# Kernel tuning notes

Hardware: AMD Instinct MI355X
Metric: run time of the kernel (lower is better)

Reference implementation:

```python
import jax, jax.numpy as jnp
import numpy as np

D_MODEL, D_HEAD, N_HEAD = 1024, 64, 16
B, T1, T2 = 2, 2048, 2048


def setup_inputs() -> dict:
    key = jax.random.key(0)
    ks = jax.random.split(key, 8)
    s = 1.0 / np.sqrt(D_MODEL)
    return {
        "x": jax.random.normal(ks[0], (B, T1, D_MODEL), dtype=jnp.float32),
        "context": jax.random.normal(ks[1], (B, T2, D_MODEL), dtype=jnp.float32),
        "bias": jax.random.normal(ks[2], (T1, T2), dtype=jnp.float32),
        "W_q": jax.random.normal(ks[3], (D_MODEL, N_HEAD * D_HEAD), dtype=jnp.float32) * s,
        "W_k": jax.random.normal(ks[4], (D_MODEL, N_HEAD * D_HEAD), dtype=jnp.float32) * s,
        "W_v": jax.random.normal(ks[5], (D_MODEL, N_HEAD * D_HEAD), dtype=jnp.float32) * s,
        "W_out": jax.random.normal(ks[6], (N_HEAD * D_HEAD, D_MODEL), dtype=jnp.float32) * s,
        "b_out": jnp.zeros((D_MODEL,), dtype=jnp.float32),
    }


def reference(x, context, bias, W_q, W_k, W_v, W_out, b_out):
    Bq, T1_, _ = x.shape
    T2_ = context.shape[1]
    atten_scale = 1.0 / np.sqrt(D_HEAD)
    # fixed (non-trainable) per-head scale: 2^{-1}, ..., 2^{-n_head}
    head_scale = jnp.exp2(-jnp.arange(1, N_HEAD + 1, dtype=jnp.float32))

    # projections -> [B, H, T, d]
    q = (x @ W_q).reshape(Bq, T1_, N_HEAD, D_HEAD).transpose(0, 2, 1, 3)
    k = (context @ W_k).reshape(Bq, T2_, N_HEAD, D_HEAD).transpose(0, 2, 1, 3)
    v = (context @ W_v).reshape(Bq, T2_, N_HEAD, D_HEAD).transpose(0, 2, 1, 3)

    # scores: [B, H, T1, T2]
    scores = jnp.einsum("bhqd,bhkd->bhqk", q, k) * atten_scale
    scores = scores + bias[None, None, :, :] * head_scale[None, :, None, None]
    attn = jax.nn.softmax(scores, axis=-1)

    out = jnp.einsum("bhqk,bhkd->bqhd", attn, v).reshape(Bq, T1_, N_HEAD * D_HEAD)
    # dropout is identity in eval mode
    return out @ W_out + b_out
```

## Files before the change

kernel.cpp:

```cpp
#include <hip/hip_runtime.h>

typedef float  f32x4   __attribute__((ext_vector_type(4)));
typedef float  f32x16  __attribute__((ext_vector_type(16)));
typedef __bf16 bf16x8  __attribute__((ext_vector_type(8)));
typedef __bf16 bf16x2  __attribute__((ext_vector_type(2)));
typedef short  short8v __attribute__((ext_vector_type(8)));
typedef unsigned uint4v __attribute__((ext_vector_type(4)));

__device__ __forceinline__ short f2bf(float f) {
  unsigned u = __float_as_uint(f);
  unsigned r = (u + 0x7FFFu + ((u >> 16) & 1u)) >> 16;
  return (short)r;
}

__device__ __forceinline__ float exp2_native(float x) {
#if __has_builtin(__builtin_amdgcn_exp2f)
  return __builtin_amdgcn_exp2f(x);
#else
  float r;
  asm("v_exp_f32 %0, %1" : "=v"(r) : "v"(x));
  return r;
#endif
}

__device__ __forceinline__ f32x4 mfma16(bf16x8 a, bf16x8 b, f32x4 c) {
  return __builtin_amdgcn_mfma_f32_16x16x32_bf16(a, b, c, 0, 0, 0);
}
__device__ __forceinline__ f32x16 mfma32(bf16x8 a, bf16x8 b, f32x16 c) {
  return __builtin_amdgcn_mfma_f32_32x32x16_bf16(a, b, c, 0, 0, 0);
}

__device__ __forceinline__ void gload16(const void* g, void* l) {
  __builtin_amdgcn_global_load_lds(
      (const __attribute__((address_space(1))) unsigned int*)g,
      (__attribute__((address_space(3))) unsigned int*)l,
      16, 0, 0);
}

__device__ __forceinline__ bf16x8 p_exchange(const unsigned* pk, int a, int hi) {
  unsigned y1 = hi ? pk[4 * a + 0] : pk[4 * a + 2];
  unsigned z1 = __shfl_xor(y1, 32);
  unsigned y2 = hi ? pk[4 * a + 1] : pk[4 * a + 3];
  unsigned z2 = __shfl_xor(y2, 32);
  unsigned w0 = hi ? z1 : pk[4 * a + 0];
  unsigned w1 = hi ? z2 : pk[4 * a + 1];
  unsigned w2 = hi ? pk[4 * a + 2] : z1;
  unsigned w3 = hi ? pk[4 * a + 3] : z2;
  uint4v q4 = {w0, w1, w2, w3};
  return __builtin_bit_cast(bf16x8, q4);
}


__global__ __launch_bounds__(256) void cvt_copy(const float* __restrict__ in,
                                                short* __restrict__ out, int n4) {
  int i = blockIdx.x * blockDim.x + threadIdx.x;
  int stride = gridDim.x * blockDim.x;
  for (; i < n4; i += stride) {
    float4 v = *(const float4*)&in[i * 4];
    short4 o;
    o.x = f2bf(v.x); o.y = f2bf(v.y); o.z = f2bf(v.z); o.w = f2bf(v.w);
    *(short4*)&out[i * 4] = o;
  }
}

__global__ __launch_bounds__(256) void cvt_bias_frag(const float* __restrict__ bias,
                                                     short* __restrict__ frag) {
  __shared__ short lb[2][2][64][8];
  int kt = blockIdx.x, w4 = blockIdx.y, Qi = blockIdx.z;
  int t = threadIdx.x;
  int row = t >> 3;
  int c0 = (t & 7) * 8;
  const float* src = bias + (size_t)(Qi * 128 + w4 * 32 + row) * 2048 + kt * 64 + c0;
  float4 v0 = *(const float4*)(src + 0);
  float4 v1 = *(const float4*)(src + 4);
  float vv[8] = {v0.x, v0.y, v0.z, v0.w, v1.x, v1.y, v1.z, v1.w};
#pragma unroll
  for (int j = 0; j < 8; j++) {
    int kc64 = c0 + j;
    int s = kc64 >> 5, kc5 = kc64 & 31;
    int hi = (kc5 >> 2) & 1, a = kc5 & 3, bq = kc5 >> 3;
    int half = bq >> 1, idx = a + 4 * (bq & 1);
    lb[s][half][hi * 32 + row][idx] = f2bf(vv[j]);
  }
  __syncthreads();
  short8v val = ((const short8v*)&lb[0][0][0][0])[t];
  size_t base = ((size_t)((Qi * 4 + w4) * 32 + kt)) * 2048;
  *(short8v*)&frag[base + t * 8] = val;
}

__global__ __launch_bounds__(256) void cvt_transpose4(const float* __restrict__ W0,
                                                      const float* __restrict__ W1,
                                                      const float* __restrict__ W2,
                                                      const float* __restrict__ W3,
                                                      short* __restrict__ T0,
                                                      short* __restrict__ T1,
                                                      short* __restrict__ T2,
                                                      short* __restrict__ T3) {
  __shared__ short t_s[64][72];
  int z = blockIdx.z;
  const float* W = (z == 0) ? W0 : (z == 1) ? W1 : (z == 2) ? W2 : W3;
  short* Wt = (z == 0) ? T0 : (z == 1) ? T1 : (z == 2) ? T2 : T3;
  int k0 = blockIdx.y * 64, n0 = blockIdx.x * 64;
  int tid = threadIdx.x;
#pragma unroll
  for (int i = 0; i < 4; i++) {
    int idx = i * 256 + tid;
    int r = idx >> 4, cg = idx & 15;
    float4 v = *(const float4*)&W[(k0 + r) * 1024 + n0 + cg * 4];
    t_s[cg * 4 + 0][r] = f2bf(v.x);
    t_s[cg * 4 + 1][r] = f2bf(v.y);
    t_s[cg * 4 + 2][r] = f2bf(v.z);
    t_s[cg * 4 + 3][r] = f2bf(v.w);
  }
  __syncthreads();
#pragma unroll
  for (int i = 0; i < 2; i++) {
    int idx = i * 256 + tid;
    int r = idx >> 3, cg = idx & 7;
    short8v val = *(short8v*)&t_s[r][cg * 8];
    *(short8v*)&Wt[(n0 + r) * 1024 + k0 + cg * 8] = val;
  }
}

template <int EPI>
__global__ __launch_bounds__(256, 4) void gemm_bf16(const short* __restrict__ A,
                                                    const short* __restrict__ Bt,
                                                    void* __restrict__ out,
                                                    void* __restrict__ out2,
                                                    const float* __restrict__ bout) {
  constexpr int KD = 1024;
  constexpr int NB = (EPI == 3) ? 32 : 16;
  __shared__ short a_s[64][64];
  __shared__ short b_s[64][64];
  int tid = threadIdx.x, w = tid >> 6, lane = tid & 63;
  int g = lane >> 4, c16 = lane & 15;
  int hsw = c16 & 7;

  int lin = blockIdx.x + NB * blockIdx.y;
  int wk = (lin & 7) * (NB * 8) + (lin >> 3);
  int c0 = (wk & (NB - 1)) * 64, r0 = (wk / NB) * 64;

  int wr = (w >> 1) * 32, wc = (w & 1) * 32;
  f32x4 acc[2][2] = {};

  for (int kt = 0; kt < KD / 64; ++kt) {
    int k0 = kt * 64;
    __syncthreads();
#pragma unroll
    for (int i = 0; i < 2; i++) {
      int cb = i * 256 + w * 64;
      int c = cb + lane;
      int row = c >> 3, kg = c & 7;
      int sw = (kg ^ (row & 7)) * 8;
      gload16(A + (r0 + row) * KD + k0 + sw, (char*)a_s + cb * 16);
      gload16(Bt + (c0 + row) * KD + k0 + sw, (char*)b_s + cb * 16);
    }
    __syncthreads();
#pragma unroll
    for (int kk = 0; kk < 2; kk++) {
      bf16x8 af[2], bf[2];
      int sl0 = ((4 * kk + g) ^ hsw) * 8;
#pragma unroll
      for (int m = 0; m < 2; m++) af[m] = *(const bf16x8*)&a_s[wr + m * 16 + c16][sl0];
#pragma unroll
      for (int n = 0; n < 2; n++) bf[n] = *(const bf16x8*)&b_s[wc + n * 16 + c16][sl0];
#pragma unroll
      for (int m = 0; m < 2; m++)
#pragma unroll
        for (int n = 0; n < 2; n++) acc[m][n] = mfma16(af[m], bf[n], acc[m][n]);
    }
  }

#pragma unroll
  for (int m = 0; m < 2; m++)
#pragma unroll
    for (int n = 0; n < 2; n++)
#pragma unroll
      for (int r = 0; r < 4; r++) {
        int row = r0 + wr + m * 16 + g * 4 + r;
        int col = c0 + wc + n * 16 + c16;
        float v = acc[m][n][r];
        int b = row >> 11, t = row & 2047;
        if (EPI == 2) {
          ((float*)out)[row * 1024 + col] = v + bout[col];
        } else if (EPI == 0) {
          int h = col >> 6, d = col & 63;
          ((short*)out)[(((b * 16 + h) * 2048) + t) * 64 + d] = f2bf(v);
        } else {
          if (col < 1024) {
            int h = col >> 6, d = col & 63;
            ((short*)out)[(((b * 16 + h) * 2048) + t) * 64 + d] = f2bf(v);
          } else {
            int cv = col - 1024;
            int h = cv >> 6, d = cv & 63;
            ((short*)out2)[(((b * 16 + h) * 64) + d) * 2048 + t] = f2bf(v);
          }
        }
      }
}

__global__ __launch_bounds__(512, 4) void flash_attn(const short* __restrict__ Qg,
                                                     const short* __restrict__ Kg,
                                                     const short* __restrict__ Vtg,
                                                     const short* __restrict__ bfrag,
                                                     short* __restrict__ Og) {
  __shared__ short k_s[2][2][64][64];
  __shared__ short v_s[2][2][64][64];

  int tid = threadIdx.x, w = tid >> 6, lane = tid & 63;
  int gid = w >> 2, w4 = w & 3;
  int hi = lane >> 5, ll = lane & 31, l7 = ll & 7;

  int lin = blockIdx.x + 16 * (blockIdx.y + 16 * blockIdx.z);
  int wk = (lin & 7) * 64 + (lin >> 3);
  int Qi = wk & 15;
  int qb = Qi * 128;
  int h = (wk >> 4) & 15;
  int b = wk >> 8;

  const short* Qh = Qg + (size_t)(b * 16 + h) * 2048 * 64;
  const short* Kh = Kg + (size_t)(b * 16 + h) * 2048 * 64;
  const short* Vh = Vtg + (size_t)(b * 16 + h) * 64 * 2048;

  const float C1 = 0.125f * 1.44269504f;
  const float C2 = exp2f(-(float)(h + 1)) * 1.44269504f;

  int qrow = qb + w4 * 32 + ll;
  const short* bw = bfrag + ((size_t)(Qi * 4 + w4) * 32) * 2048 + lane * 8;

  int srow = tid >> 3, st8 = tid & 7;
  int ssw = (st8 ^ (srow & 7)) * 8;

  {
    gload16(Kh + srow * 64 + ssw, (char*)&k_s[0][0][0][0] + w * 64 * 16);
    gload16(Vh + srow * 2048 + ssw, (char*)&v_s[0][0][0][0] + w * 64 * 16);
    gload16(Kh + 64 * 64 + srow * 64 + ssw, (char*)&k_s[0][1][0][0] + w * 64 * 16);
    gload16(Vh + srow * 2048 + 64 + ssw, (char*)&v_s[0][1][0][0] + w * 64 * 16);
  }
  bf16x8 bvA[4];
#pragma unroll
  for (int j = 0; j < 4; j++)
    bvA[j] = *(const bf16x8*)(bw + (size_t)gid * 2048 + j * 512);
  bf16x8 qf[4];
#pragma unroll
  for (int dm = 0; dm < 4; dm++)
    qf[dm] = *(const bf16x8*)(Qh + (size_t)qrow * 64 + dm * 16 + hi * 8);
  asm volatile("" ::: "memory");

  float l0 = 0.f, l1 = 0.f, l2 = 0.f, l3 = 0.f;
  f32x16 o_acc[2] = {};

  for (int r = 0; r < 16; ++r) {
    int cur = r & 1;
    int kt = 2 * r + gid;

    bf16x8 bvB[4];
    if (r < 15) {
#pragma unroll
      for (int j = 0; j < 4; j++)
        bvB[j] = *(const bf16x8*)(bw + (size_t)(kt + 2) * 2048 + j * 512);
      int tA = 2 * r + 2;
      gload16(Kh + (size_t)tA * 4096 + srow * 64 + ssw,
              (char*)&k_s[cur ^ 1][0][0][0] + w * 64 * 16);
      gload16(Vh + srow * 2048 + tA * 64 + ssw,
              (char*)&v_s[cur ^ 1][0][0][0] + w * 64 * 16);
      gload16(Kh + (size_t)(tA + 1) * 4096 + srow * 64 + ssw,
              (char*)&k_s[cur ^ 1][1][0][0] + w * 64 * 16);
      gload16(Vh + srow * 2048 + (tA + 1) * 64 + ssw,
              (char*)&v_s[cur ^ 1][1][0][0] + w * 64 * 16);
      asm volatile("s_waitcnt vmcnt(8)" ::: "memory");
    } else {
      asm volatile("s_waitcnt vmcnt(0)" ::: "memory");
    }
    __builtin_amdgcn_s_barrier();

    f32x16 sacc = {};
#pragma unroll
    for (int dm = 0; dm < 4; dm++) {
      const short* kr = &k_s[cur][gid][ll][((2 * dm + hi) ^ l7) * 8];
      sacc = mfma32(*(const bf16x8*)kr, qf[dm], sacc);
    }

    unsigned pk[8];
#pragma unroll
    for (int i = 0; i < 8; i++) {
      float b0 = (float)(i < 4 ? bvA[0][2 * i] : bvA[1][2 * i - 8]);
      float b1 = (float)(i < 4 ? bvA[0][2 * i + 1] : bvA[1][2 * i - 7]);
      float p0 = exp2_native(sacc[2 * i] * C1 + b0 * C2);
      float p1 = exp2_native(sacc[2 * i + 1] * C1 + b1 * C2);
      l0 += p0; l1 += p1;
      bf16x2 pp = {(__bf16)p0, (__bf16)p1};
      pk[i] = __builtin_bit_cast(unsigned, pp);
    }

#pragma unroll
    for (int a = 0; a < 2; a++) {
      bf16x8 PA = p_exchange(pk, a, hi);
#pragma unroll
      for (int dt = 0; dt < 2; dt++) {
        const short* vr = &v_s[cur][gid][dt * 32 + ll][((2 * a + hi) ^ l7) * 8];
        o_acc[dt] = mfma32(PA, *(const bf16x8*)vr, o_acc[dt]);
      }
    }
    asm volatile("" ::: "memory");

    f32x16 sacc1 = {};
#pragma unroll
    for (int dm = 0; dm < 4; dm++) {
      const short* kr = &k_s[cur][gid][32 + ll][((2 * dm + hi) ^ l7) * 8];
      sacc1 = mfma32(*(const bf16x8*)kr, qf[dm], sacc1);
    }

#pragma unroll
    for (int i = 0; i < 8; i++) {
      float b0 = (float)(i < 4 ? bvA[2][2 * i] : bvA[3][2 * i - 8]);
      float b1 = (float)(i < 4 ? bvA[2][2 * i + 1] : bvA[3][2 * i - 7]);
      float p0 = exp2_native(sacc1[2 * i] * C1 + b0 * C2);
      float p1 = exp2_native(sacc1[2 * i + 1] * C1 + b1 * C2);
      l2 += p0; l3 += p1;
      bf16x2 pp = {(__bf16)p0, (__bf16)p1};
      pk[i] = __builtin_bit_cast(unsigned, pp);
    }

#pragma unroll
    for (int a = 0; a < 2; a++) {
      bf16x8 PA = p_exchange(pk, a, hi);
#pragma unroll
      for (int dt = 0; dt < 2; dt++) {
        const short* vr = &v_s[cur][gid][dt * 32 + ll][((4 + 2 * a + hi) ^ l7) * 8];
        o_acc[dt] = mfma32(PA, *(const bf16x8*)vr, o_acc[dt]);
      }
    }
    __builtin_amdgcn_s_barrier();

#pragma unroll
    for (int j = 0; j < 4; j++) bvA[j] = bvB[j];
  }

  float l_run = (l0 + l1) + (l2 + l3);

  l_run += __shfl_xor(l_run, 32);
  float* ox = (float*)&k_s[0][0][0][0];
  float* lx = (float*)&v_s[0][0][0][0];
  if (gid == 1) {
#pragma unroll
    for (int k = 0; k < 32; k++)
      ox[(w4 * 32 + k) * 64 + lane] = o_acc[k >> 4][k & 15];
    if (lane < 32) lx[w4 * 32 + lane] = l_run;
  }
  __syncthreads();
  if (gid == 0) {
    float invl = 1.f / (l_run + lx[w4 * 32 + ll]);
#pragma unroll
    for (int k = 0; k < 32; k++)
      o_acc[k >> 4][k & 15] += ox[(w4 * 32 + k) * 64 + lane];

#pragma unroll
    for (int r = 0; r < 16; r++) {
      int q = (r & 3) + 8 * (r >> 2) + 4 * hi;
      float iv = __shfl(invl, q);
      int tg = qb + w4 * 32 + q;
#pragma unroll
      for (int dt = 0; dt < 2; dt++) {
        Og[(size_t)(b * 2048 + tg) * 1024 + h * 64 + dt * 32 + ll] =
            f2bf(o_acc[dt][r] * iv);
      }
    }
  }
}

extern "C" void kernel_launch(void* const* d_in, const int* in_sizes, int n_in,
                              void* d_out, int out_size, void* d_ws, size_t ws_size,
                              hipStream_t stream) {
  const float* x    = (const float*)d_in[0];
  const float* ctx  = (const float*)d_in[1];
  const float* bias = (const float*)d_in[2];
  const float* Wq   = (const float*)d_in[3];
  const float* Wk   = (const float*)d_in[4];
  const float* Wv   = (const float*)d_in[5];
  const float* Wo   = (const float*)d_in[6];
  const float* bo   = (const float*)d_in[7];
  float* out = (float*)d_out;

  char* ws = (char*)d_ws;
  short* x_bf = (short*)(ws + 0);
  short* c_bf = (short*)(ws + 8388608);
  short* wq_t = (short*)(ws + 16777216);
  short* wk_t = (short*)(ws + 18874368);
  short* wv_t = (short*)(ws + 20971520);
  short* wo_t = (short*)(ws + 23068672);
  short* q_ws = (short*)(ws + 25165824);
  short* k_ws = (short*)(ws + 33554432);
  short* v_ws = (short*)(ws + 41943040);
  short* o_ws = (short*)(ws + 50331648);
  short* bias_fr = x_bf;

  cvt_copy<<<1024, 256, 0, stream>>>(x, x_bf, 1048576);
  cvt_copy<<<1024, 256, 0, stream>>>(ctx, c_bf, 1048576);
  dim3 tg(16, 16, 4);
  cvt_transpose4<<<tg, 256, 0, stream>>>(Wq, Wk, Wv, Wo, wq_t, wk_t, wv_t, wo_t);

  dim3 gq(16, 64);
  gemm_bf16<0><<<gq, 256, 0, stream>>>(x_bf, wq_t, q_ws, nullptr, nullptr);
  dim3 gkv(32, 64);
  gemm_bf16<3><<<gkv, 256, 0, stream>>>(c_bf, wk_t, k_ws, v_ws, nullptr);

  dim3 bg(32, 4, 16);
  cvt_bias_frag<<<bg, 256, 0, stream>>>(bias, bias_fr);

  dim3 fg(16, 16, 2);
  flash_attn<<<fg, 512, 0, stream>>>(q_ws, k_ws, v_ws, bias_fr, o_ws);

  gemm_bf16<2><<<gq, 256, 0, stream>>>(o_ws, wo_t, out, nullptr, bo);
}
```

Before: 174.3 us.

## Merge Q and KV projections into one 128x128-tile GEMM and reorder attention MFMAs

Replaces the two separate Q and KV projection launches with a single gemm_qkv kernel that uses 128x128 tiles (4x4 MFMA tiles per wave) and covers both projections in one 768-block grid. The aim is more operand reuse per LDS load and one fewer launch. The output GEMM becomes its own specialised kernel. In flash attention, the second QK^T MFMA chain is issued before the first PV MFMAs so matrix work can overlap the exp computation. The larger tiles raise register and LDS use (launch bounds drop to 3 blocks per SM), and the kernel relies on wk_t and wv_t sitting next to each other in the workspace.

```diff
diff --git a/kernel.cpp b/kernel.cpp
--- a/kernel.cpp
+++ b/kernel.cpp
@@ -122,23 +122,96 @@
   }
 }
 
-template <int EPI>
-__global__ __launch_bounds__(256, 4) void gemm_bf16(const short* __restrict__ A,
-                                                    const short* __restrict__ Bt,
-                                                    void* __restrict__ out,
-                                                    void* __restrict__ out2,
-                                                    const float* __restrict__ bout) {
+__global__ __launch_bounds__(256, 3) void gemm_qkv(const short* __restrict__ x_bf,
+                                                   const short* __restrict__ c_bf,
+                                                   const short* __restrict__ wq_t,
+                                                   const short* __restrict__ wkv_t,
+                                                   short* __restrict__ q_ws,
+                                                   short* __restrict__ k_ws,
+                                                   short* __restrict__ v_ws) {
+  __shared__ short a_s[128][64];
+  __shared__ short b_s[128][64];
+  int tid = threadIdx.x, w = tid >> 6, lane = tid & 63;
+  int g = lane >> 4, c16 = lane & 15, hsw = c16 & 7;
+
+  int lin = blockIdx.x;
+  int wk = (lin & 7) * 96 + (lin >> 3);
+  bool isQ = wk < 256;
+  int t0 = isQ ? wk : wk - 256;
+  int nt = isQ ? 8 : 16;
+  int c0 = (t0 % nt) * 128, r0 = (t0 / nt) * 128;
+  const short* A  = isQ ? x_bf : c_bf;
+  const short* Bt = isQ ? wq_t : wkv_t;
+
+  int wr = (w >> 1) * 64, wc = (w & 1) * 64;
+  f32x4 acc[4][4] = {};
+
+  for (int kt = 0; kt < 16; ++kt) {
+    int k0 = kt * 64;
+    __syncthreads();
+#pragma unroll
+    for (int i = 0; i < 4; i++) {
+      int cb = i * 256 + w * 64;
+      int c = cb + lane;
+      int row = c >> 3, kg = c & 7;
+      int sw = (kg ^ (row & 7)) * 8;
+      gload16(A + (size_t)(r0 + row) * 1024 + k0 + sw, (char*)a_s + cb * 16);
+      gload16(Bt + (size_t)(c0 + row) * 1024 + k0 + sw, (char*)b_s + cb * 16);
+    }
+    __syncthreads();
+#pragma unroll
+    for (int kk = 0; kk < 2; kk++) {
+      bf16x8 af[4], bf[4];
+      int sl0 = ((4 * kk + g) ^ hsw) * 8;
+#pragma unroll
+      for (int m = 0; m < 4; m++) af[m] = *(const bf16x8*)&a_s[wr + m * 16 + c16][sl0];
+#pragma unroll
+      for (int n = 0; n < 4; n++) bf[n] = *(const bf16x8*)&b_s[wc + n * 16 + c16][sl0];
+#pragma unroll
+      for (int m = 0; m < 4; m++)
+#pragma unroll
+        for (int n = 0; n < 4; n++) acc[m][n] = mfma16(af[m], bf[n], acc[m][n]);
+    }
+  }
+
+#pragma unroll
+  for (int m = 0; m < 4; m++)
+#pragma unroll
+    for (int n = 0; n < 4; n++)
+#pragma unroll
+      for (int r = 0; r < 4; r++) {
+        int row = r0 + wr + m * 16 + g * 4 + r;
+        int col = c0 + wc + n * 16 + c16;
+        short bv = f2bf(acc[m][n][r]);
+        int b = row >> 11, t = row & 2047;
+        if (isQ) {
+          int h = col >> 6, d = col & 63;
+          q_ws[(((b * 16 + h) * 2048) + t) * 64 + d] = bv;
+        } else if (col < 1024) {
+          int h = col >> 6, d = col & 63;
+          k_ws[(((b * 16 + h) * 2048) + t) * 64 + d] = bv;
+        } else {
+          int cv = col - 1024;
+          int h = cv >> 6, d = cv & 63;
+          v_ws[(((b * 16 + h) * 64) + d) * 2048 + t] = bv;
+        }
+      }
+}
+
+__global__ __launch_bounds__(256, 4) void gemm_out(const short* __restrict__ A,
+                                                   const short* __restrict__ Bt,
+                                                   float* __restrict__ out,
+                                                   const float* __restrict__ bout) {
   constexpr int KD = 1024;
-  constexpr int NB = (EPI == 3) ? 32 : 16;
   __shared__ short a_s[64][64];
   __shared__ short b_s[64][64];
   int tid = threadIdx.x, w = tid >> 6, lane = tid & 63;
   int g = lane >> 4, c16 = lane & 15;
   int hsw = c16 & 7;
 
-  int lin = blockIdx.x + NB * blockIdx.y;
-  int wk = (lin & 7) * (NB * 8) + (lin >> 3);
-  int c0 = (wk & (NB - 1)) * 64, r0 = (wk / NB) * 64;
+  int lin = blockIdx.x + 16 * blockIdx.y;
+  int wk = (lin & 7) * 128 + (lin >> 3);
+  int c0 = (wk & 15) * 64, r0 = (wk >> 4) * 64;
 
   int wr = (w >> 1) * 32, wc = (w & 1) * 32;
   f32x4 acc[2][2] = {};
@@ -179,23 +252,7 @@
       for (int r = 0; r < 4; r++) {
         int row = r0 + wr + m * 16 + g * 4 + r;
         int col = c0 + wc + n * 16 + c16;
-        float v = acc[m][n][r];
-        int b = row >> 11, t = row & 2047;
-        if (EPI == 2) {
-          ((float*)out)[row * 1024 + col] = v + bout[col];
-        } else if (EPI == 0) {
-          int h = col >> 6, d = col & 63;
-          ((short*)out)[(((b * 16 + h) * 2048) + t) * 64 + d] = f2bf(v);
-        } else {
-          if (col < 1024) {
-            int h = col >> 6, d = col & 63;
-            ((short*)out)[(((b * 16 + h) * 2048) + t) * 64 + d] = f2bf(v);
-          } else {
-            int cv = col - 1024;
-            int h = cv >> 6, d = cv & 63;
-            ((short*)out2)[(((b * 16 + h) * 64) + d) * 2048 + t] = f2bf(v);
-          }
-        }
+        out[row * 1024 + col] = acc[m][n][r] + bout[col];
       }
 }
 
@@ -281,7 +338,7 @@
       sacc = mfma32(*(const bf16x8*)kr, qf[dm], sacc);
     }
 
-    unsigned pk[8];
+    unsigned pk0[8];
 #pragma unroll
     for (int i = 0; i < 8; i++) {
       float b0 = (float)(i < 4 ? bvA[0][2 * i] : bvA[1][2 * i - 8]);
@@ -290,27 +347,29 @@
       float p1 = exp2_native(sacc[2 * i + 1] * C1 + b1 * C2);
       l0 += p0; l1 += p1;
       bf16x2 pp = {(__bf16)p0, (__bf16)p1};
-      pk[i] = __builtin_bit_cast(unsigned, pp);
-    }
+      pk0[i] = __builtin_bit_cast(unsigned, pp);
+    }
+    asm volatile("" ::: "memory");
+
+    f32x16 sacc1 = {};
+#pragma unroll
+    for (int dm = 0; dm < 4; dm++) {
+      const short* kr = &k_s[cur][gid][32 + ll][((2 * dm + hi) ^ l7) * 8];
+      sacc1 = mfma32(*(const bf16x8*)kr, qf[dm], sacc1);
+    }
+    asm volatile("" ::: "memory");
 
 #pragma unroll
     for (int a = 0; a < 2; a++) {
-      bf16x8 PA = p_exchange(pk, a, hi);
+      bf16x8 PA = p_exchange(pk0, a, hi);
 #pragma unroll
       for (int dt = 0; dt < 2; dt++) {
         const short* vr = &v_s[cur][gid][dt * 32 + ll][((2 * a + hi) ^ l7) * 8];
         o_acc[dt] = mfma32(PA, *(const bf16x8*)vr, o_acc[dt]);
       }
     }
-    asm volatile("" ::: "memory");
-
-    f32x16 sacc1 = {};
-#pragma unroll
-    for (int dm = 0; dm < 4; dm++) {
-      const short* kr = &k_s[cur][gid][32 + ll][((2 * dm + hi) ^ l7) * 8];
-      sacc1 = mfma32(*(const bf16x8*)kr, qf[dm], sacc1);
-    }
-
+
+    unsigned pk1[8];
 #pragma unroll
     for (int i = 0; i < 8; i++) {
       float b0 = (float)(i < 4 ? bvA[2][2 * i] : bvA[3][2 * i - 8]);
@@ -319,12 +378,12 @@
       float p1 = exp2_native(sacc1[2 * i + 1] * C1 + b1 * C2);
       l2 += p0; l3 += p1;
       bf16x2 pp = {(__bf16)p0, (__bf16)p1};
-      pk[i] = __builtin_bit_cast(unsigned, pp);
+      pk1[i] = __builtin_bit_cast(unsigned, pp);
     }
 
 #pragma unroll
     for (int a = 0; a < 2; a++) {
-      bf16x8 PA = p_exchange(pk, a, hi);
+      bf16x8 PA = p_exchange(pk1, a, hi);
 #pragma unroll
       for (int dt = 0; dt < 2; dt++) {
         const short* vr = &v_s[cur][gid][dt * 32 + ll][((4 + 2 * a + hi) ^ l7) * 8];
@@ -400,10 +459,7 @@
   dim3 tg(16, 16, 4);
   cvt_transpose4<<<tg, 256, 0, stream>>>(Wq, Wk, Wv, Wo, wq_t, wk_t, wv_t, wo_t);
 
-  dim3 gq(16, 64);
-  gemm_bf16<0><<<gq, 256, 0, stream>>>(x_bf, wq_t, q_ws, nullptr, nullptr);
-  dim3 gkv(32, 64);
-  gemm_bf16<3><<<gkv, 256, 0, stream>>>(c_bf, wk_t, k_ws, v_ws, nullptr);
+  gemm_qkv<<<768, 256, 0, stream>>>(x_bf, c_bf, wq_t, wk_t, q_ws, k_ws, v_ws);
 
   dim3 bg(32, 4, 16);
   cvt_bias_frag<<<bg, 256, 0, stream>>>(bias, bias_fr);
@@ -411,5 +467,6 @@
   dim3 fg(16, 16, 2);
   flash_attn<<<fg, 512, 0, stream>>>(q_ws, k_ws, v_ws, bias_fr, o_ws);
 
-  gemm_bf16<2><<<gq, 256, 0, stream>>>(o_ws, wo_t, out, nullptr, bo);
-}
+  dim3 go(16, 64);
+  gemm_out<<<go, 256, 0, stream>>>(o_ws, wo_t, out, bo);
+}
```

New measurement: 166.5 us. 4.5% less time.
